# Kernel optimization log

Hardware: AMD Instinct MI355X
Metric: run time of the kernel (lower is better)

Reference implementation:

```python
import jax, jax.numpy as jnp
import numpy as np
import math

DIM = 1024
NUM_HEADS = 16
QUANTUM_HEADS = 2
HEAD_DIM = DIM // NUM_HEADS          # 64
TRAD_HEADS = NUM_HEADS - QUANTUM_HEADS  # 14
B, S = 1, 1024
STEPS = 2048
LN_EPS = 1e-5


def setup_inputs() -> dict:
    key = jax.random.key(0)
    ks = jax.random.split(key, 10)
    hd2 = 2 * HEAD_DIM
    return {
        "x": jax.random.normal(ks[0], (B, S, DIM), jnp.float32),
        # to_quantum_state: Linear(head_dim -> 2*head_dim) + LayerNorm + Tanh (shared across quantum heads)
        "qs_W": jax.random.normal(ks[1], (hd2, HEAD_DIM), jnp.float32) / math.sqrt(HEAD_DIM),
        "qs_b": jnp.zeros((hd2,), jnp.float32),
        "ln_g": jnp.ones((hd2,), jnp.float32),
        "ln_b": jnp.zeros((hd2,), jnp.float32),
        # per-quantum-head scalars
        "q_freq": jax.random.normal(ks[2], (QUANTUM_HEADS,), jnp.float32) * 0.02,
        "q_shift": jax.random.normal(ks[3], (QUANTUM_HEADS,), jnp.float32) * 0.02,
        # traditional head projections (no bias)
        "Wq": jax.random.normal(ks[4], (TRAD_HEADS * HEAD_DIM, DIM), jnp.float32) / math.sqrt(DIM),
        "Wk": jax.random.normal(ks[5], (TRAD_HEADS * HEAD_DIM, DIM), jnp.float32) / math.sqrt(DIM),
        "Wv": jax.random.normal(ks[6], (TRAD_HEADS * HEAD_DIM, DIM), jnp.float32) / math.sqrt(DIM),
        # output projection (with bias)
        "Wo": jax.random.normal(ks[7], (DIM, DIM), jnp.float32) / math.sqrt(DIM),
        "bo": jnp.zeros((DIM,), jnp.float32),
    }


def _layernorm(h, g, b):
    mu = jnp.mean(h, axis=-1, keepdims=True)
    var = jnp.mean(jnp.square(h - mu), axis=-1, keepdims=True)
    return (h - mu) * jax.lax.rsqrt(var + LN_EPS) * g + b


def _forward(x, qs_W, qs_b, ln_g, ln_b, q_freq, q_shift, Wq, Wk, Wv, Wo, bo):
    cos_table = jnp.cos(jnp.linspace(0.0, 2.0 * math.pi, STEPS).astype(jnp.float32))
    scale = 1.0 / math.sqrt(HEAD_DIM)
    two_pi = 2.0 * math.pi

    outs = []
    # ---- quantum heads (small fixed loop over structurally distinct heads) ----
    for h in range(QUANTUM_HEADS):
        xh = x[..., h * HEAD_DIM:(h + 1) * HEAD_DIM]          # (B,S,hd)
        qs = jnp.tanh(_layernorm(xh @ qs_W.T + qs_b, ln_g, ln_b))  # (B,S,2hd)
        amp, phase = jnp.split(qs, 2, axis=-1)                 # each (B,S,hd)
        # per (query pos i, key pos j, feature d) phase difference
        pd = (phase[:, :, None, :] - phase[:, None, :, :]) * q_freq[h] + q_shift[h]  # (B,S,S,hd)
        idx = jnp.floor(jnp.mod(pd / two_pi * STEPS, STEPS)).astype(jnp.int32)
        interf = cos_table[idx]                                # lookup-table gather, (B,S,S,hd)
        attn = jnp.einsum('bid,bjd,bijd->bij', amp, amp, interf) * scale
        attn = jax.nn.softmax(attn, axis=-1)
        outs.append(attn @ xh)                                 # (B,S,hd), values are the raw head slice

    # ---- traditional heads: standard multi-head attention ----
    q = (x @ Wq.T).reshape(B, S, TRAD_HEADS, HEAD_DIM)
    k = (x @ Wk.T).reshape(B, S, TRAD_HEADS, HEAD_DIM)
    v = (x @ Wv.T).reshape(B, S, TRAD_HEADS, HEAD_DIM)
    scores = jnp.einsum('bqhd,bkhd->bhqk', q, k) * scale       # (B,Ht,S,S)
    probs = jax.nn.softmax(scores, axis=-1)
    trad = jnp.einsum('bhqk,bkhd->bqhd', probs, v).reshape(B, S, TRAD_HEADS * HEAD_DIM)
    outs.append(trad)

    out = jnp.concatenate(outs, axis=-1)                       # (B,S,DIM)
    return out @ Wo.T + bo


def reference(x, qs_W, qs_b, ln_g, ln_b, q_freq, q_shift, Wq, Wk, Wv, Wo, bo):
    return _forward(x, qs_W, qs_b, ln_g, ln_b, q_freq, q_shift, Wq, Wk, Wv, Wo, bo)
```

## Files before the change

kernel.cpp:

```cpp
#include <hip/hip_runtime.h>
#include <hip/hip_bf16.h>
#include <math.h>

#define DIMX 1024
#define SEQ  1024
#define HD   64
#define QH   2
#define TH   14
#define QKVN 2688
#define LN_EPS 1e-5f

typedef __bf16 bf16x8 __attribute__((ext_vector_type(8)));
typedef float  f32x4  __attribute__((ext_vector_type(4)));
typedef unsigned short u16x8 __attribute__((ext_vector_type(8)));

__device__ inline unsigned short f2b_rne(float f) {
  unsigned int u = __float_as_uint(f);
  unsigned int r = (u + 0x7FFF + ((u >> 16) & 1)) >> 16;
  return (unsigned short)r;
}

__device__ inline float waveRedSum(float v) {
  #pragma unroll
  for (int off = 32; off; off >>= 1) v += __shfl_xor(v, off, 64);
  return v;
}

__global__ __launch_bounds__(256) void k_f2b_all(
    const float* __restrict__ x, const float* __restrict__ wq,
    const float* __restrict__ wk, const float* __restrict__ wv,
    const float* __restrict__ wo,
    unsigned short* __restrict__ x_bf, unsigned short* __restrict__ wqkv_bf,
    unsigned short* __restrict__ wo_bf) {
  long i = ((long)blockIdx.x * 256 + threadIdx.x) * 4;
  float4 v;
  unsigned short* dst;
  if (i < 1048576) {
    v = *reinterpret_cast<const float4*>(x + i);
    dst = x_bf + i;
  } else if (i < 3801088) {
    long j = i - 1048576;
    const float* s = (j < 917504) ? wq + j
                   : (j < 1835008) ? wk + (j - 917504)
                                   : wv + (j - 1835008);
    v = *reinterpret_cast<const float4*>(s);
    dst = wqkv_bf + j;
  } else {
    long j = i - 3801088;
    v = *reinterpret_cast<const float4*>(wo + j);
    dst = wo_bf + j;
  }
  ushort4 o;
  o.x = f2b_rne(v.x); o.y = f2b_rne(v.y); o.z = f2b_rne(v.z); o.w = f2b_rne(v.w);
  *reinterpret_cast<ushort4*>(dst) = o;
}

__global__ __launch_bounds__(128) void k_qprep(
    const float* __restrict__ x, const float* __restrict__ qsW,
    const float* __restrict__ qsb, const float* __restrict__ lng,
    const float* __restrict__ lnb, const float* __restrict__ qfreq,
    const float* __restrict__ qshift,
    unsigned short* __restrict__ qcs, unsigned short* __restrict__ kcs) {
  int b = blockIdx.x; int h = b >> 10; int i = b & 1023;
  int o = threadIdx.x;
  __shared__ float xrow[HD];
  __shared__ float red[4];
  __shared__ float qsv[128];
  if (o < HD) xrow[o] = x[i * DIMX + h * HD + o];
  __syncthreads();
  float s = qsb[o];
  #pragma unroll
  for (int d = 0; d < HD; d += 4) {
    float4 w = *reinterpret_cast<const float4*>(qsW + o * HD + d);
    float4 xv = *reinterpret_cast<const float4*>(&xrow[d]);
    s += xv.x * w.x + xv.y * w.y + xv.z * w.z + xv.w * w.w;
  }
  int wid = o >> 6, lane = o & 63;
  float ws = waveRedSum(s);
  if (lane == 0) red[wid] = ws;
  __syncthreads();
  float mu = (red[0] + red[1]) * (1.0f / 128.0f);
  float dv = s - mu;
  float ws2 = waveRedSum(dv * dv);
  if (lane == 0) red[2 + wid] = ws2;
  __syncthreads();
  float var = (red[2] + red[3]) * (1.0f / 128.0f);
  float y = dv * rsqrtf(var + LN_EPS) * lng[o] + lnb[o];
  qsv[o] = tanhf(y);
  __syncthreads();
  float freq = qfreq[h], shift = qshift[h];
  size_t base = ((size_t)h * 1024 + i) * 128;
  if (o < HD) {
    float amp = qsv[o];
    float a = qsv[64 + o] * freq + shift;
    float sn, cs;
    __sincosf(a, &sn, &cs);
    qcs[base + o]      = f2b_rne(amp * cs);
    qcs[base + 64 + o] = f2b_rne(amp * sn);
  } else {
    int d = o - 64;
    float amp = qsv[d];
    float bAng = qsv[64 + d] * freq;
    float sn, cs;
    __sincosf(bAng, &sn, &cs);
    kcs[base + d]      = f2b_rne(amp * cs);
    kcs[base + 64 + d] = f2b_rne(amp * sn);
  }
}

__global__ __launch_bounds__(256) void k_tr64all(
    const unsigned short* __restrict__ qkv, const unsigned short* __restrict__ xb,
    unsigned short* __restrict__ vt, unsigned short* __restrict__ xt) {
  int hy = blockIdx.y, kv0 = blockIdx.x * 64;
  const unsigned short* src;
  unsigned short* dst;
  int ld, col0;
  if (hy < TH) { src = qkv; ld = QKVN; col0 = 1792 + hy * 64; dst = vt + (size_t)hy * 65536; }
  else         { src = xb;  ld = DIMX; col0 = (hy - TH) * 64; dst = xt + (size_t)(hy - TH) * 65536; }
  int t = threadIdx.x;
  __shared__ unsigned short tile[64][72];
  #pragma unroll
  for (int pass = 0; pass < 2; ++pass) {
    int s = pass * 256 + t;
    int r = s >> 3, c8 = (s & 7) * 8;
    u16x8 v = *reinterpret_cast<const u16x8*>(src + (size_t)(kv0 + r) * ld + col0 + c8);
    *reinterpret_cast<u16x8*>(&tile[r][c8]) = v;
  }
  __syncthreads();
  #pragma unroll
  for (int pass = 0; pass < 2; ++pass) {
    int s = pass * 256 + t;
    int d = s >> 3, k8 = (s & 7) * 8;
    u16x8 o;
    #pragma unroll
    for (int j = 0; j < 8; ++j) o[j] = tile[k8 + j][d];
    *reinterpret_cast<u16x8*>(dst + (size_t)d * 1024 + kv0 + k8) = o;
  }
}

template <int DQK, int NT>
__global__ __launch_bounds__(256) void k_fattn(
    const unsigned short* __restrict__ Qb, long q_hstep, int ldq,
    const unsigned short* __restrict__ Kb, long k_hstep, int ldk,
    const unsigned short* __restrict__ Vtb, long v_hstep, int slot0,
    float* __restrict__ pout, float* __restrict__ pml) {
  const int LQ = DQK + 8;
  const int KREG = DQK / 32;
  __shared__ unsigned short Qs[64 * LQ];
  __shared__ unsigned short Ks[2][64 * LQ];
  __shared__ unsigned short Vs[2][64 * 72];
  __shared__ unsigned short Ps[64 * 72];
  int h = blockIdx.y;
  int q0 = blockIdx.x * 64;
  int split = blockIdx.z;
  int kv0 = split * (NT * 64);
  int t = threadIdx.x, lane = t & 63, w = t >> 6;
  int g = lane >> 4, li = lane & 15;
  const unsigned short* Qp = Qb + (size_t)h * q_hstep;
  const unsigned short* Kp = Kb + (size_t)h * k_hstep;
  const unsigned short* Vp = Vtb + (size_t)h * v_hstep;

  #pragma unroll
  for (int i = 0; i < DQK / 32; ++i) {
    int s = i * 64 + lane;
    int r = s / (DQK / 8), c8 = (s % (DQK / 8)) * 8;
    u16x8 v = *reinterpret_cast<const u16x8*>(Qp + (size_t)(q0 + w * 16 + r) * ldq + c8);
    *reinterpret_cast<u16x8*>(&Qs[(w * 16 + r) * LQ + c8]) = v;
  }

  u16x8 kreg[KREG], vreg[2];
  auto loadKV = [&](int tile) {
    int j0 = kv0 + tile * 64;
    #pragma unroll
    for (int i = 0; i < KREG; ++i) {
      int s = i * 256 + t;
      int r = s / (DQK / 8), c8 = (s % (DQK / 8)) * 8;
      kreg[i] = *reinterpret_cast<const u16x8*>(Kp + (size_t)(j0 + r) * ldk + c8);
    }
    #pragma unroll
    for (int i = 0; i < 2; ++i) {
      int s = i * 256 + t;
      int d = s >> 3, c8 = (s & 7) * 8;
      vreg[i] = *reinterpret_cast<const u16x8*>(Vp + (size_t)d * 1024 + j0 + c8);
    }
  };
  auto writeKV = [&](int buf) {
    #pragma unroll
    for (int i = 0; i < KREG; ++i) {
      int s = i * 256 + t;
      int r = s / (DQK / 8), c8 = (s % (DQK / 8)) * 8;
      *reinterpret_cast<u16x8*>(&Ks[buf][r * LQ + c8]) = kreg[i];
    }
    #pragma unroll
    for (int i = 0; i < 2; ++i) {
      int s = i * 256 + t;
      int d = s >> 3, c8 = (s & 7) * 8;
      *reinterpret_cast<u16x8*>(&Vs[buf][d * 72 + c8]) = vreg[i];
    }
  };

  loadKV(0);
  writeKV(0);
  loadKV(1);
  __syncthreads();

  f32x4 acc_o[4] = {};
  float mrow[4] = {-1e30f, -1e30f, -1e30f, -1e30f};
  float lrow[4] = {0.f, 0.f, 0.f, 0.f};

  #pragma unroll
  for (int tile = 0; tile < NT; ++tile) {
    int cur = tile & 1;
    if (tile < NT - 1) writeKV(cur ^ 1);
    if (tile < NT - 2) loadKV(tile + 2);
    f32x4 s_acc[4] = {};
    #pragma unroll
    for (int kk = 0; kk < DQK / 32; ++kk) {
      bf16x8 aq = *reinterpret_cast<const bf16x8*>(&Qs[(w * 16 + li) * LQ + kk * 32 + g * 8]);
      #pragma unroll
      for (int n = 0; n < 4; ++n) {
        bf16x8 bk = *reinterpret_cast<const bf16x8*>(&Ks[cur][(n * 16 + li) * LQ + kk * 32 + g * 8]);
        s_acc[n] = __builtin_amdgcn_mfma_f32_16x16x32_bf16(aq, bk, s_acc[n], 0, 0, 0);
      }
    }
    #pragma unroll
    for (int r = 0; r < 4; ++r) {
      float tm = fmaxf(fmaxf(s_acc[0][r], s_acc[1][r]), fmaxf(s_acc[2][r], s_acc[3][r]));
      #pragma unroll
      for (int m = 1; m < 16; m <<= 1) tm = fmaxf(tm, __shfl_xor(tm, m, 64));
      float mn = fmaxf(mrow[r], tm);
      float sf = __expf((mrow[r] - mn) * 0.125f);
      mrow[r] = mn;
      lrow[r] *= sf;
      #pragma unroll
      for (int n = 0; n < 4; ++n) acc_o[n][r] *= sf;
      float rs = 0.f;
      #pragma unroll
      for (int n = 0; n < 4; ++n) {
        float p = __expf((s_acc[n][r] - mn) * 0.125f);
        s_acc[n][r] = p;
        rs += p;
      }
      #pragma unroll
      for (int m = 1; m < 16; m <<= 1) rs += __shfl_xor(rs, m, 64);
      lrow[r] += rs;
    }
    #pragma unroll
    for (int n = 0; n < 4; ++n)
      #pragma unroll
      for (int r = 0; r < 4; ++r)
        Ps[(w * 16 + g * 4 + r) * 72 + n * 16 + li] = f2b_rne(s_acc[n][r]);
    #pragma unroll
    for (int kk = 0; kk < 2; ++kk) {
      bf16x8 ap = *reinterpret_cast<const bf16x8*>(&Ps[(w * 16 + li) * 72 + kk * 32 + g * 8]);
      #pragma unroll
      for (int n = 0; n < 4; ++n) {
        bf16x8 bv = *reinterpret_cast<const bf16x8*>(&Vs[cur][(n * 16 + li) * 72 + kk * 32 + g * 8]);
        acc_o[n] = __builtin_amdgcn_mfma_f32_16x16x32_bf16(ap, bv, acc_o[n], 0, 0, 0);
      }
    }
    __syncthreads();
  }

  size_t rowbase = (size_t)(slot0 + h * gridDim.z + split) * 1024;
  #pragma unroll
  for (int r = 0; r < 4; ++r) {
    int qr = q0 + w * 16 + g * 4 + r;
    #pragma unroll
    for (int n = 0; n < 4; ++n)
      pout[(rowbase + qr) * 64 + n * 16 + li] = acc_o[n][r];
    if (li == 0) {
      pml[(rowbase + qr) * 2 + 0] = mrow[r];
      pml[(rowbase + qr) * 2 + 1] = lrow[r];
    }
  }
}

__global__ __launch_bounds__(256) void k_fmerge(
    const float* __restrict__ pout, const float* __restrict__ pml,
    unsigned short* __restrict__ concat) {
  int rq = blockIdx.x * 4 + (threadIdx.x >> 6);
  int lh = rq >> 10, q = rq & 1023;
  int d = threadIdx.x & 63;
  int s0 = (lh < 2) ? lh * 8 : 16 + (lh - 2) * 4;
  int ns = (lh < 2) ? 8 : 4;
  float m_s[8], l_s[8];
  float M = -1e30f;
  #pragma unroll
  for (int s = 0; s < 8; ++s) {
    if (s < ns) {
      size_t rb = (size_t)(s0 + s) * 1024 + q;
      m_s[s] = pml[rb * 2 + 0];
      l_s[s] = pml[rb * 2 + 1];
      M = fmaxf(M, m_s[s]);
    }
  }
  float num = 0.f, den = 0.f;
  #pragma unroll
  for (int s = 0; s < 8; ++s) {
    if (s < ns) {
      float wgt = __expf((m_s[s] - M) * 0.125f);
      num += wgt * pout[((size_t)(s0 + s) * 1024 + q) * 64 + d];
      den += wgt * l_s[s];
    }
  }
  concat[(size_t)q * DIMX + lh * 64 + d] = f2b_rne(num / den);
}

template <int HAS_BIAS, int BF16_OUT>
__global__ __launch_bounds__(256) void k_gemm64s(
    const unsigned short* __restrict__ A, const unsigned short* __restrict__ B,
    void* __restrict__ Cv, const float* __restrict__ bias,
    int K, int lda, int ldb, int ldc) {
  __shared__ unsigned short As[64 * 64];
  __shared__ unsigned short Bs[64 * 64];
  int t = threadIdx.x, lane = t & 63, w = t >> 6;
  int wr = w >> 1, wc = w & 1;
  int g = lane >> 4, li = lane & 15;
  int mb = blockIdx.y * 64, nb = blockIdx.x * 64;
  int rstg = t >> 3;
  int cswz = (((t & 7) ^ (rstg & 7)) * 8);
  f32x4 acc[2][2] = {};
  for (int kb = 0; kb < K; kb += 64) {
    __syncthreads();
    #pragma unroll
    for (int i = 0; i < 2; ++i) {
      __builtin_amdgcn_global_load_lds(
          (const __attribute__((address_space(1))) unsigned int*)(A + (size_t)(mb + i * 32 + rstg) * lda + kb + cswz),
          (__attribute__((address_space(3))) unsigned int*)(As + i * 2048 + t * 8), 16, 0, 0);
      __builtin_amdgcn_global_load_lds(
          (const __attribute__((address_space(1))) unsigned int*)(B + (size_t)(nb + i * 32 + rstg) * ldb + kb + cswz),
          (__attribute__((address_space(3))) unsigned int*)(Bs + i * 2048 + t * 8), 16, 0, 0);
    }
    __syncthreads();
    #pragma unroll
    for (int kk = 0; kk < 2; ++kk) {
      bf16x8 af[2], bfr[2];
      #pragma unroll
      for (int m = 0; m < 2; ++m) {
        int r = wr * 32 + m * 16 + li;
        int cb = kk * 4 + g;
        af[m] = *reinterpret_cast<const bf16x8*>(&As[r * 64 + ((cb ^ (r & 7)) * 8)]);
      }
      #pragma unroll
      for (int n = 0; n < 2; ++n) {
        int r = wc * 32 + n * 16 + li;
        int cb = kk * 4 + g;
        bfr[n] = *reinterpret_cast<const bf16x8*>(&Bs[r * 64 + ((cb ^ (r & 7)) * 8)]);
      }
      #pragma unroll
      for (int m = 0; m < 2; ++m)
        #pragma unroll
        for (int n = 0; n < 2; ++n)
          acc[m][n] = __builtin_amdgcn_mfma_f32_16x16x32_bf16(af[m], bfr[n], acc[m][n], 0, 0, 0);
    }
  }
  #pragma unroll
  for (int m = 0; m < 2; ++m) {
    int row0 = mb + wr * 32 + m * 16 + g * 4;
    #pragma unroll
    for (int n = 0; n < 2; ++n) {
      int col = nb + wc * 32 + n * 16 + li;
      float bval = HAS_BIAS ? bias[col] : 0.0f;
      #pragma unroll
      for (int r = 0; r < 4; ++r) {
        size_t idx = (size_t)(row0 + r) * ldc + col;
        if (BF16_OUT) ((unsigned short*)Cv)[idx] = f2b_rne(acc[m][n][r] + bval);
        else          ((float*)Cv)[idx] = acc[m][n][r] + bval;
      }
    }
  }
}

extern "C" void kernel_launch(void* const* d_in, const int* in_sizes, int n_in,
                              void* d_out, int out_size, void* d_ws, size_t ws_size,
                              hipStream_t stream) {
  const float* x      = (const float*)d_in[0];
  const float* qsW    = (const float*)d_in[1];
  const float* qsb    = (const float*)d_in[2];
  const float* lng    = (const float*)d_in[3];
  const float* lnb    = (const float*)d_in[4];
  const float* qfreq  = (const float*)d_in[5];
  const float* qshift = (const float*)d_in[6];
  const float* Wq     = (const float*)d_in[7];
  const float* Wk     = (const float*)d_in[8];
  const float* Wv     = (const float*)d_in[9];
  const float* Wo     = (const float*)d_in[10];
  const float* bo     = (const float*)d_in[11];
  float* out = (float*)d_out;

  char* ws = (char*)d_ws;
  size_t off = 0;
  auto alloc = [&](size_t bytes) { char* p = ws + off; off += (bytes + 255) & ~(size_t)255; return p; };
  unsigned short* x_bf      = (unsigned short*)alloc((size_t)SEQ * DIMX * 2);
  unsigned short* wqkv_bf   = (unsigned short*)alloc((size_t)QKVN * DIMX * 2);
  unsigned short* wo_bf     = (unsigned short*)alloc((size_t)DIMX * DIMX * 2);
  unsigned short* concat_bf = (unsigned short*)alloc((size_t)SEQ * DIMX * 2);
  unsigned short* qkv_bf    = (unsigned short*)alloc((size_t)SEQ * QKVN * 2);
  unsigned short* qcs       = (unsigned short*)alloc((size_t)QH * SEQ * 128 * 2);
  unsigned short* kcs       = (unsigned short*)alloc((size_t)QH * SEQ * 128 * 2);
  unsigned short* vt        = (unsigned short*)alloc((size_t)TH * HD * SEQ * 2);
  unsigned short* xt        = (unsigned short*)alloc((size_t)QH * HD * SEQ * 2);
  float*          pout      = (float*)alloc((size_t)72 * SEQ * 64 * 4);
  float*          pml       = (float*)alloc((size_t)72 * SEQ * 2 * 4);

  k_f2b_all<<<4736, 256, 0, stream>>>(x, Wq, Wk, Wv, Wo, x_bf, wqkv_bf, wo_bf);
  k_qprep<<<QH * SEQ, 128, 0, stream>>>(x, qsW, qsb, lng, lnb, qfreq, qshift, qcs, kcs);

  k_gemm64s<0, 1><<<dim3(QKVN / 64, SEQ / 64), 256, 0, stream>>>(
      x_bf, wqkv_bf, qkv_bf, nullptr, DIMX, DIMX, DIMX, QKVN);

  k_tr64all<<<dim3(16, 16), 256, 0, stream>>>(qkv_bf, x_bf, vt, xt);

  k_fattn<128, 2><<<dim3(16, QH, 8), 256, 0, stream>>>(
      qcs, (long)SEQ * 128, 128, kcs, (long)SEQ * 128, 128, xt, (long)HD * SEQ, 0, pout, pml);
  k_fattn<64, 4><<<dim3(16, TH, 4), 256, 0, stream>>>(
      qkv_bf, 64, QKVN, qkv_bf + 896, 64, QKVN, vt, (long)HD * SEQ, 16, pout, pml);
  k_fmerge<<<16 * SEQ / 4, 256, 0, stream>>>(pout, pml, concat_bf);

  k_gemm64s<1, 0><<<dim3(DIMX / 64, SEQ / 64), 256, 0, stream>>>(
      concat_bf, wo_bf, out, bo, DIMX, DIMX, DIMX, DIMX);
}
```

Measured before the change: 81.53 us.

## Merge prep kernels, fuse V transpose into QKV GEMM epilogue, unify attention launches

```diff
diff --git a/kernel.cpp b/kernel.cpp
--- a/kernel.cpp
+++ b/kernel.cpp
@@ -9,6 +9,9 @@
 #define TH   14
 #define QKVN 2688
 #define LN_EPS 1e-5f
+#define NB_F2B 4736
+#define NB_QPREP 1024
+#define NB_XT 32
 
 typedef __bf16 bf16x8 __attribute__((ext_vector_type(8)));
 typedef float  f32x4  __attribute__((ext_vector_type(4)));
@@ -26,139 +29,137 @@
   return v;
 }
 
-__global__ __launch_bounds__(256) void k_f2b_all(
-    const float* __restrict__ x, const float* __restrict__ wq,
-    const float* __restrict__ wk, const float* __restrict__ wv,
-    const float* __restrict__ wo,
-    unsigned short* __restrict__ x_bf, unsigned short* __restrict__ wqkv_bf,
-    unsigned short* __restrict__ wo_bf) {
-  long i = ((long)blockIdx.x * 256 + threadIdx.x) * 4;
-  float4 v;
-  unsigned short* dst;
-  if (i < 1048576) {
-    v = *reinterpret_cast<const float4*>(x + i);
-    dst = x_bf + i;
-  } else if (i < 3801088) {
-    long j = i - 1048576;
-    const float* s = (j < 917504) ? wq + j
-                   : (j < 1835008) ? wk + (j - 917504)
-                                   : wv + (j - 1835008);
-    v = *reinterpret_cast<const float4*>(s);
-    dst = wqkv_bf + j;
-  } else {
-    long j = i - 3801088;
-    v = *reinterpret_cast<const float4*>(wo + j);
-    dst = wo_bf + j;
-  }
-  ushort4 o;
-  o.x = f2b_rne(v.x); o.y = f2b_rne(v.y); o.z = f2b_rne(v.z); o.w = f2b_rne(v.w);
-  *reinterpret_cast<ushort4*>(dst) = o;
-}
-
-__global__ __launch_bounds__(128) void k_qprep(
+__global__ __launch_bounds__(256) void k_prep(
     const float* __restrict__ x, const float* __restrict__ qsW,
     const float* __restrict__ qsb, const float* __restrict__ lng,
     const float* __restrict__ lnb, const float* __restrict__ qfreq,
     const float* __restrict__ qshift,
-    unsigned short* __restrict__ qcs, unsigned short* __restrict__ kcs) {
-  int b = blockIdx.x; int h = b >> 10; int i = b & 1023;
-  int o = threadIdx.x;
-  __shared__ float xrow[HD];
-  __shared__ float red[4];
-  __shared__ float qsv[128];
-  if (o < HD) xrow[o] = x[i * DIMX + h * HD + o];
-  __syncthreads();
-  float s = qsb[o];
-  #pragma unroll
-  for (int d = 0; d < HD; d += 4) {
-    float4 w = *reinterpret_cast<const float4*>(qsW + o * HD + d);
-    float4 xv = *reinterpret_cast<const float4*>(&xrow[d]);
-    s += xv.x * w.x + xv.y * w.y + xv.z * w.z + xv.w * w.w;
-  }
-  int wid = o >> 6, lane = o & 63;
-  float ws = waveRedSum(s);
-  if (lane == 0) red[wid] = ws;
-  __syncthreads();
-  float mu = (red[0] + red[1]) * (1.0f / 128.0f);
-  float dv = s - mu;
-  float ws2 = waveRedSum(dv * dv);
-  if (lane == 0) red[2 + wid] = ws2;
-  __syncthreads();
-  float var = (red[2] + red[3]) * (1.0f / 128.0f);
-  float y = dv * rsqrtf(var + LN_EPS) * lng[o] + lnb[o];
-  qsv[o] = tanhf(y);
-  __syncthreads();
-  float freq = qfreq[h], shift = qshift[h];
-  size_t base = ((size_t)h * 1024 + i) * 128;
-  if (o < HD) {
-    float amp = qsv[o];
-    float a = qsv[64 + o] * freq + shift;
-    float sn, cs;
-    __sincosf(a, &sn, &cs);
-    qcs[base + o]      = f2b_rne(amp * cs);
-    qcs[base + 64 + o] = f2b_rne(amp * sn);
+    const float* __restrict__ wq, const float* __restrict__ wk,
+    const float* __restrict__ wv, const float* __restrict__ wo,
+    unsigned short* __restrict__ x_bf, unsigned short* __restrict__ wqkv_bf,
+    unsigned short* __restrict__ wo_bf,
+    unsigned short* __restrict__ qcs, unsigned short* __restrict__ kcs,
+    unsigned short* __restrict__ xt) {
+  __shared__ float xrow2[2][HD];
+  __shared__ float redm[2][2], redv[2][2];
+  __shared__ float qsv2[2][128];
+  __shared__ unsigned short ttile[64][72];
+  int t = threadIdx.x;
+  int bid = blockIdx.x;
+  if (bid < NB_F2B) {
+    long i = ((long)bid * 256 + t) * 4;
+    float4 v;
+    unsigned short* dst;
+    if (i < 1048576) {
+      v = *reinterpret_cast<const float4*>(x + i);
+      dst = x_bf + i;
+    } else if (i < 3801088) {
+      long j = i - 1048576;
+      const float* s = (j < 917504) ? wq + j
+                     : (j < 1835008) ? wk + (j - 917504)
+                                     : wv + (j - 1835008);
+      v = *reinterpret_cast<const float4*>(s);
+      dst = wqkv_bf + j;
+    } else {
+      long j = i - 3801088;
+      v = *reinterpret_cast<const float4*>(wo + j);
+      dst = wo_bf + j;
+    }
+    ushort4 o;
+    o.x = f2b_rne(v.x); o.y = f2b_rne(v.y); o.z = f2b_rne(v.z); o.w = f2b_rne(v.w);
+    *reinterpret_cast<ushort4*>(dst) = o;
+  } else if (bid < NB_F2B + NB_QPREP) {
+    int half = t >> 7, o = t & 127;
+    int row = (bid - NB_F2B) * 2 + half;
+    int h = row >> 10, i = row & 1023;
+    if (o < HD) xrow2[half][o] = x[i * DIMX + h * HD + o];
+    __syncthreads();
+    float s = qsb[o];
+    #pragma unroll
+    for (int d = 0; d < HD; d += 4) {
+      float4 w = *reinterpret_cast<const float4*>(qsW + o * HD + d);
+      float4 xv = *reinterpret_cast<const float4*>(&xrow2[half][d]);
+      s += xv.x * w.x + xv.y * w.y + xv.z * w.z + xv.w * w.w;
+    }
+    int wid = (o >> 6), lane = o & 63;
+    float ws = waveRedSum(s);
+    if (lane == 0) redm[half][wid] = ws;
+    __syncthreads();
+    float mu = (redm[half][0] + redm[half][1]) * (1.0f / 128.0f);
+    float dv = s - mu;
+    float ws2 = waveRedSum(dv * dv);
+    if (lane == 0) redv[half][wid] = ws2;
+    __syncthreads();
+    float var = (redv[half][0] + redv[half][1]) * (1.0f / 128.0f);
+    float y = dv * rsqrtf(var + LN_EPS) * lng[o] + lnb[o];
+    qsv2[half][o] = tanhf(y);
+    __syncthreads();
+    float freq = qfreq[h], shift = qshift[h];
+    size_t base = ((size_t)h * 1024 + i) * 128;
+    if (o < HD) {
+      float amp = qsv2[half][o];
+      float a = qsv2[half][64 + o] * freq + shift;
+      float sn, cs;
+      __sincosf(a, &sn, &cs);
+      qcs[base + o]      = f2b_rne(amp * cs);
+      qcs[base + 64 + o] = f2b_rne(amp * sn);
+    } else {
+      int d = o - 64;
+      float amp = qsv2[half][d];
+      float bAng = qsv2[half][64 + d] * freq;
+      float sn, cs;
+      __sincosf(bAng, &sn, &cs);
+      kcs[base + d]      = f2b_rne(amp * cs);
+      kcs[base + 64 + d] = f2b_rne(amp * sn);
+    }
   } else {
-    int d = o - 64;
-    float amp = qsv[d];
-    float bAng = qsv[64 + d] * freq;
-    float sn, cs;
-    __sincosf(bAng, &sn, &cs);
-    kcs[base + d]      = f2b_rne(amp * cs);
-    kcs[base + 64 + d] = f2b_rne(amp * sn);
-  }
-}
-
-__global__ __launch_bounds__(256) void k_tr64all(
-    const unsigned short* __restrict__ qkv, const unsigned short* __restrict__ xb,
-    unsigned short* __restrict__ vt, unsigned short* __restrict__ xt) {
-  int hy = blockIdx.y, kv0 = blockIdx.x * 64;
-  const unsigned short* src;
-  unsigned short* dst;
-  int ld, col0;
-  if (hy < TH) { src = qkv; ld = QKVN; col0 = 1792 + hy * 64; dst = vt + (size_t)hy * 65536; }
-  else         { src = xb;  ld = DIMX; col0 = (hy - TH) * 64; dst = xt + (size_t)(hy - TH) * 65536; }
-  int t = threadIdx.x;
-  __shared__ unsigned short tile[64][72];
-  #pragma unroll
-  for (int pass = 0; pass < 2; ++pass) {
-    int s = pass * 256 + t;
-    int r = s >> 3, c8 = (s & 7) * 8;
-    u16x8 v = *reinterpret_cast<const u16x8*>(src + (size_t)(kv0 + r) * ld + col0 + c8);
-    *reinterpret_cast<u16x8*>(&tile[r][c8]) = v;
-  }
-  __syncthreads();
-  #pragma unroll
-  for (int pass = 0; pass < 2; ++pass) {
-    int s = pass * 256 + t;
-    int d = s >> 3, k8 = (s & 7) * 8;
-    u16x8 o;
-    #pragma unroll
-    for (int j = 0; j < 8; ++j) o[j] = tile[k8 + j][d];
-    *reinterpret_cast<u16x8*>(dst + (size_t)d * 1024 + kv0 + k8) = o;
+    int b = bid - (NB_F2B + NB_QPREP);
+    int h = b >> 4, kv0 = (b & 15) * 64;
+    #pragma unroll
+    for (int pass = 0; pass < 2; ++pass) {
+      int s = pass * 256 + t;
+      int r = s >> 3, c8 = (s & 7) * 8;
+      const float* src = x + (size_t)(kv0 + r) * DIMX + h * 64 + c8;
+      float4 a = *reinterpret_cast<const float4*>(src);
+      float4 b4 = *reinterpret_cast<const float4*>(src + 4);
+      ushort4 o1, o2;
+      o1.x = f2b_rne(a.x);  o1.y = f2b_rne(a.y);  o1.z = f2b_rne(a.z);  o1.w = f2b_rne(a.w);
+      o2.x = f2b_rne(b4.x); o2.y = f2b_rne(b4.y); o2.z = f2b_rne(b4.z); o2.w = f2b_rne(b4.w);
+      *reinterpret_cast<ushort4*>(&ttile[r][c8]) = o1;
+      *reinterpret_cast<ushort4*>(&ttile[r][c8 + 4]) = o2;
+    }
+    __syncthreads();
+    #pragma unroll
+    for (int pass = 0; pass < 2; ++pass) {
+      int s = pass * 256 + t;
+      int d = s >> 3, k8 = (s & 7) * 8;
+      u16x8 o;
+      #pragma unroll
+      for (int j = 0; j < 8; ++j) o[j] = ttile[k8 + j][d];
+      *reinterpret_cast<u16x8*>(xt + (size_t)h * 65536 + (size_t)d * 1024 + kv0 + k8) = o;
+    }
   }
 }
 
 template <int DQK, int NT>
-__global__ __launch_bounds__(256) void k_fattn(
-    const unsigned short* __restrict__ Qb, long q_hstep, int ldq,
-    const unsigned short* __restrict__ Kb, long k_hstep, int ldk,
-    const unsigned short* __restrict__ Vtb, long v_hstep, int slot0,
+__device__ __forceinline__ void dev_fattn(
+    char* smem,
+    const unsigned short* __restrict__ Qp, int ldq,
+    const unsigned short* __restrict__ Kp, int ldk,
+    const unsigned short* __restrict__ Vp,
+    int q0, int split, int slot,
     float* __restrict__ pout, float* __restrict__ pml) {
   const int LQ = DQK + 8;
   const int KREG = DQK / 32;
-  __shared__ unsigned short Qs[64 * LQ];
-  __shared__ unsigned short Ks[2][64 * LQ];
-  __shared__ unsigned short Vs[2][64 * 72];
-  __shared__ unsigned short Ps[64 * 72];
-  int h = blockIdx.y;
-  int q0 = blockIdx.x * 64;
-  int split = blockIdx.z;
+  unsigned short* Qs  = (unsigned short*)smem;
+  unsigned short* Ks0 = Qs + 64 * LQ;
+  unsigned short* Ks1 = Ks0 + 64 * LQ;
+  unsigned short* Vs0 = Ks1 + 64 * LQ;
+  unsigned short* Vs1 = Vs0 + 64 * 72;
+  unsigned short* Ps  = Vs1 + 64 * 72;
   int kv0 = split * (NT * 64);
   int t = threadIdx.x, lane = t & 63, w = t >> 6;
   int g = lane >> 4, li = lane & 15;
-  const unsigned short* Qp = Qb + (size_t)h * q_hstep;
-  const unsigned short* Kp = Kb + (size_t)h * k_hstep;
-  const unsigned short* Vp = Vtb + (size_t)h * v_hstep;
 
   #pragma unroll
   for (int i = 0; i < DQK / 32; ++i) {
@@ -185,23 +186,25 @@
     }
   };
   auto writeKV = [&](int buf) {
+    unsigned short* Ksb = buf ? Ks1 : Ks0;
+    unsigned short* Vsb = buf ? Vs1 : Vs0;
     #pragma unroll
     for (int i = 0; i < KREG; ++i) {
       int s = i * 256 + t;
       int r = s / (DQK / 8), c8 = (s % (DQK / 8)) * 8;
-      *reinterpret_cast<u16x8*>(&Ks[buf][r * LQ + c8]) = kreg[i];
+      *reinterpret_cast<u16x8*>(&Ksb[r * LQ + c8]) = kreg[i];
     }
     #pragma unroll
     for (int i = 0; i < 2; ++i) {
       int s = i * 256 + t;
       int d = s >> 3, c8 = (s & 7) * 8;
-      *reinterpret_cast<u16x8*>(&Vs[buf][d * 72 + c8]) = vreg[i];
+      *reinterpret_cast<u16x8*>(&Vsb[d * 72 + c8]) = vreg[i];
     }
   };
 
   loadKV(0);
   writeKV(0);
-  loadKV(1);
+  if (NT > 1) loadKV(1);
   __syncthreads();
 
   f32x4 acc_o[4] = {};
@@ -211,6 +214,8 @@
   #pragma unroll
   for (int tile = 0; tile < NT; ++tile) {
     int cur = tile & 1;
+    unsigned short* Ksc = cur ? Ks1 : Ks0;
+    unsigned short* Vsc = cur ? Vs1 : Vs0;
     if (tile < NT - 1) writeKV(cur ^ 1);
     if (tile < NT - 2) loadKV(tile + 2);
     f32x4 s_acc[4] = {};
@@ -219,7 +224,7 @@
       bf16x8 aq = *reinterpret_cast<const bf16x8*>(&Qs[(w * 16 + li) * LQ + kk * 32 + g * 8]);
       #pragma unroll
       for (int n = 0; n < 4; ++n) {
-        bf16x8 bk = *reinterpret_cast<const bf16x8*>(&Ks[cur][(n * 16 + li) * LQ + kk * 32 + g * 8]);
+        bf16x8 bk = *reinterpret_cast<const bf16x8*>(&Ksc[(n * 16 + li) * LQ + kk * 32 + g * 8]);
         s_acc[n] = __builtin_amdgcn_mfma_f32_16x16x32_bf16(aq, bk, s_acc[n], 0, 0, 0);
       }
     }
@@ -255,14 +260,14 @@
       bf16x8 ap = *reinterpret_cast<const bf16x8*>(&Ps[(w * 16 + li) * 72 + kk * 32 + g * 8]);
       #pragma unroll
       for (int n = 0; n < 4; ++n) {
-        bf16x8 bv = *reinterpret_cast<const bf16x8*>(&Vs[cur][(n * 16 + li) * 72 + kk * 32 + g * 8]);
+        bf16x8 bv = *reinterpret_cast<const bf16x8*>(&Vsc[(n * 16 + li) * 72 + kk * 32 + g * 8]);
         acc_o[n] = __builtin_amdgcn_mfma_f32_16x16x32_bf16(ap, bv, acc_o[n], 0, 0, 0);
       }
     }
     __syncthreads();
   }
 
-  size_t rowbase = (size_t)(slot0 + h * gridDim.z + split) * 1024;
+  size_t rowbase = (size_t)slot * 1024;
   #pragma unroll
   for (int r = 0; r < 4; ++r) {
     int qr = q0 + w * 16 + g * 4 + r;
@@ -273,6 +278,28 @@
       pml[(rowbase + qr) * 2 + 0] = mrow[r];
       pml[(rowbase + qr) * 2 + 1] = lrow[r];
     }
+  }
+}
+
+__global__ __launch_bounds__(256) void k_fattn_all(
+    const unsigned short* __restrict__ qcs, const unsigned short* __restrict__ kcs,
+    const unsigned short* __restrict__ xt, const unsigned short* __restrict__ qkv,
+    const unsigned short* __restrict__ vt,
+    float* __restrict__ pout, float* __restrict__ pml) {
+  __shared__ __align__(16) char smem[79872];
+  int bid = blockIdx.x;
+  if (bid < 256) {
+    int qt = bid & 15, h = (bid >> 4) & 1, split = bid >> 5;
+    dev_fattn<128, 2>(smem, qcs + (size_t)h * SEQ * 128, 128,
+                      kcs + (size_t)h * SEQ * 128, 128,
+                      xt + (size_t)h * 65536, qt * 64, split, h * 8 + split, pout, pml);
+  } else {
+    int b2 = bid - 256;
+    int qt = b2 & 15, hs = b2 >> 4;
+    int h = hs % 14, split = hs / 14;
+    dev_fattn<64, 4>(smem, qkv + h * 64, QKVN,
+                     qkv + 896 + h * 64, QKVN,
+                     vt + (size_t)h * 65536, qt * 64, split, 16 + h * 4 + split, pout, pml);
   }
 }
 
@@ -311,6 +338,7 @@
 __global__ __launch_bounds__(256) void k_gemm64s(
     const unsigned short* __restrict__ A, const unsigned short* __restrict__ B,
     void* __restrict__ Cv, const float* __restrict__ bias,
+    unsigned short* __restrict__ vtp,
     int K, int lda, int ldb, int ldc) {
   __shared__ unsigned short As[64 * 64];
   __shared__ unsigned short Bs[64 * 64];
@@ -354,6 +382,20 @@
         for (int n = 0; n < 2; ++n)
           acc[m][n] = __builtin_amdgcn_mfma_f32_16x16x32_bf16(af[m], bfr[n], acc[m][n], 0, 0, 0);
     }
+  }
+  if (vtp != nullptr && nb >= 1792) {
+    #pragma unroll
+    for (int m = 0; m < 2; ++m) {
+      int row0 = mb + wr * 32 + m * 16 + g * 4;
+      #pragma unroll
+      for (int n = 0; n < 2; ++n) {
+        int colrel = nb - 1792 + wc * 32 + n * 16 + li;
+        #pragma unroll
+        for (int r = 0; r < 4; ++r)
+          vtp[(size_t)colrel * 1024 + row0 + r] = f2b_rne(acc[m][n][r]);
+      }
+    }
+    return;
   }
   #pragma unroll
   for (int m = 0; m < 2; ++m) {
@@ -404,20 +446,17 @@
   float*          pout      = (float*)alloc((size_t)72 * SEQ * 64 * 4);
   float*          pml       = (float*)alloc((size_t)72 * SEQ * 2 * 4);
 
-  k_f2b_all<<<4736, 256, 0, stream>>>(x, Wq, Wk, Wv, Wo, x_bf, wqkv_bf, wo_bf);
-  k_qprep<<<QH * SEQ, 128, 0, stream>>>(x, qsW, qsb, lng, lnb, qfreq, qshift, qcs, kcs);
+  k_prep<<<NB_F2B + NB_QPREP + NB_XT, 256, 0, stream>>>(
+      x, qsW, qsb, lng, lnb, qfreq, qshift, Wq, Wk, Wv, Wo,
+      x_bf, wqkv_bf, wo_bf, qcs, kcs, xt);
 
   k_gemm64s<0, 1><<<dim3(QKVN / 64, SEQ / 64), 256, 0, stream>>>(
-      x_bf, wqkv_bf, qkv_bf, nullptr, DIMX, DIMX, DIMX, QKVN);
-
-  k_tr64all<<<dim3(16, 16), 256, 0, stream>>>(qkv_bf, x_bf, vt, xt);
-
-  k_fattn<128, 2><<<dim3(16, QH, 8), 256, 0, stream>>>(
-      qcs, (long)SEQ * 128, 128, kcs, (long)SEQ * 128, 128, xt, (long)HD * SEQ, 0, pout, pml);
-  k_fattn<64, 4><<<dim3(16, TH, 4), 256, 0, stream>>>(
-      qkv_bf, 64, QKVN, qkv_bf + 896, 64, QKVN, vt, (long)HD * SEQ, 16, pout, pml);
+      x_bf, wqkv_bf, qkv_bf, nullptr, vt, DIMX, DIMX, DIMX, QKVN);
+
+  k_fattn_all<<<1152, 256, 0, stream>>>(qcs, kcs, xt, qkv_bf, vt, pout, pml);
+
   k_fmerge<<<16 * SEQ / 4, 256, 0, stream>>>(pout, pml, concat_bf);
 
   k_gemm64s<1, 0><<<dim3(DIMX / 64, SEQ / 64), 256, 0, stream>>>(
-      concat_bf, wo_bf, out, bo, DIMX, DIMX, DIMX, DIMX);
-}
+      concat_bf, wo_bf, out, bo, nullptr, DIMX, DIMX, DIMX, DIMX);
+}
```

Measured after the change: 80.71 us. Within noise of the previous version (-1.0%).
